# Kernel tuning notes

Measured on AMD Instinct MI355X. Metric: run time of the kernel, lower is better.

The kernel has to match this reference:

```python
import jax, jax.numpy as jnp
import numpy as np

VOCAB = 100000
EMBED = 64
SENT = 20
MEM = 50
BATCH = 32
HOPS = 3
PAD_ID = 0


def position_encoding(sentence_size, embedding_size):
    # Section 4.1 of MemN2N paper, vectorized. Returns [sentence_size, embedding_size].
    i = np.arange(1, embedding_size + 1, dtype=np.float32)[:, None]   # [E,1]
    j = np.arange(1, sentence_size + 1, dtype=np.float32)[None, :]    # [1,S]
    enc = (i - (embedding_size + 1) / 2.0) * (j - (sentence_size + 1) / 2.0)
    enc = 1.0 + 4.0 * enc / embedding_size / sentence_size
    enc[:, -1] = 1.0
    return jnp.asarray(enc.T, dtype=jnp.float32)  # [S,E]


def setup_inputs() -> dict:
    key = jax.random.key(0)
    k1, k2, k3, k4 = jax.random.split(key, 4)
    stories = jax.random.randint(k1, (BATCH, MEM, SENT), 0, VOCAB, dtype=jnp.int64 if jax.config.jax_enable_x64 else jnp.int32)
    queries = jax.random.randint(k2, (BATCH, SENT), 0, VOCAB, dtype=jnp.int64 if jax.config.jax_enable_x64 else jnp.int32)
    A = jax.random.normal(k3, (VOCAB, EMBED), dtype=jnp.float32) * 0.1
    C = jax.random.normal(k4, (HOPS, VOCAB, EMBED), dtype=jnp.float32) * 0.1
    # padding_idx=PAD_ID rows are zero, as in nn.Embedding(padding_idx=...)
    A = A.at[PAD_ID].set(0.0)
    C = C.at[:, PAD_ID].set(0.0)
    encoding = position_encoding(SENT, EMBED)
    return {"stories": stories, "queries": queries, "A": A, "C": C, "encoding": encoding}


def reference(stories, queries, A, C, encoding):
    # queries: [B,S], stories: [B,M,S], A: [V,E], C: [hops,V,E], encoding: [S,E]
    q_emb = A[queries]                                # [B,S,E]
    u = (q_emb * encoding).sum(axis=1)                # [B,E]
    for hop in range(HOPS):
        table_in = A if hop == 0 else C[hop - 1]
        emb_A = table_in[stories]                     # [B,M,S,E]
        m = (emb_A * encoding).sum(axis=2)            # [B,M,E]
        dotted = jnp.einsum('bme,be->bm', m, u)       # [B,M]
        probs = jax.nn.softmax(dotted, axis=-1)       # [B,M]
        emb_C = C[hop][stories]                       # [B,M,S,E]
        c = (emb_C * encoding).sum(axis=2)            # [B,M,E]
        o = jnp.einsum('bm,bme->be', probs, c)        # [B,E]
        u = u + o
    return u @ C[-1].T                                # [B,V]
```

## Files before the change

kernel.cpp:

```cpp
#include <hip/hip_runtime.h>
#include <hip/hip_bf16.h>

#define VOCAB 100000
#define EMBED 64
#define SENT  20
#define MEM   50
#define BATCH 32
#define HOPS  3

#define NSET  4
#define NSLOT (NSET * BATCH * MEM)

__device__ __forceinline__ float bfr(unsigned short x) {
    union { unsigned int u; float f; } cv;
    cv.u = ((unsigned int)x) << 16;
    return cv.f;
}

__device__ __forceinline__ bool is_bf16(const void* enc) {
    return ((const unsigned int*)enc)[639] == 0x3F803F80u;
}

__device__ __forceinline__ float loadT(const void* p, size_t idx, bool bf) {
    return bf ? bfr(((const unsigned short*)p)[idx]) : ((const float*)p)[idx];
}

__device__ __forceinline__ float wave_sum(float d) {
#pragma unroll
    for (int off = 32; off > 0; off >>= 1) d += __shfl_xor(d, off, 64);
    return d;
}

__global__ __launch_bounds__(256) void k_gather(
    const int* __restrict__ stories,
    const int* __restrict__ queries,
    const void* __restrict__ A,
    const void* __restrict__ C,
    const void* __restrict__ enc,
    float* __restrict__ mc_ws,
    float* __restrict__ u0g)
{
    const bool bf = is_bf16(enc);
    const int tid = threadIdx.x;
    const int e   = tid & 63;
    const int gw  = blockIdx.x * 4 + (tid >> 6);
    const size_t VE = (size_t)VOCAB * EMBED;

    float encr[SENT];
#pragma unroll
    for (int s = 0; s < SENT; ++s) encr[s] = loadT(enc, s * EMBED + e, bf);

    if (gw < NSLOT) {
        const int t  = gw / (BATCH * MEM);
        const int bm = gw % (BATCH * MEM);
        const void* T   = (t == 0) ? A : C;
        const size_t to = (t == 0) ? 0 : (size_t)(t - 1) * VE;

        int wst = (e < SENT) ? stories[bm * SENT + e] : 0;
        float acc = 0.f;
#pragma unroll
        for (int s = 0; s < SENT; ++s) {
            int w = __shfl(wst, s, 64);
            acc += loadT(T, to + (size_t)w * EMBED + e, bf) * encr[s];
        }
        mc_ws[gw * EMBED + e] = acc;
    } else if (gw < NSLOT + BATCH) {
        const int b = gw - NSLOT;
        int wq = (e < SENT) ? queries[b * SENT + e] : 0;
        float u = 0.f;
#pragma unroll
        for (int s = 0; s < SENT; ++s) {
            int w = __shfl(wq, s, 64);
            u += loadT(A, (size_t)w * EMBED + e, bf) * encr[s];
        }
        u0g[b * EMBED + e] = u;
    }
}

__global__ __launch_bounds__(256) void k_recur2(
    const float* __restrict__ mc_ws,
    const float* __restrict__ u0g,
    float* __restrict__ u3g)
{
    const int b    = blockIdx.x;
    const int tid  = threadIdx.x;
    const int lane = tid & 63;
    const int widx = tid >> 6;

    __shared__ float mc[NSET][MEM][65];
    __shared__ float uls[EMBED];
    __shared__ float ols[4][EMBED];

    for (int idx = tid; idx < NSET * MEM * 16; idx += 256) {
        int t  = idx / (MEM * 16);
        int r  = idx % (MEM * 16);
        int mm = r >> 4;
        int e4 = r & 15;
        const float4 v = *(const float4*)(mc_ws +
            (((size_t)t * BATCH * MEM) + (size_t)b * MEM + mm) * EMBED + e4 * 4);
        mc[t][mm][e4 * 4 + 0] = v.x;
        mc[t][mm][e4 * 4 + 1] = v.y;
        mc[t][mm][e4 * 4 + 2] = v.z;
        mc[t][mm][e4 * 4 + 3] = v.w;
    }
    if (tid < EMBED) uls[tid] = u0g[b * EMBED + tid];
    __syncthreads();

    for (int hop = 0; hop < HOPS; ++hop) {
        float d = 0.f;
        if (lane < MEM) {
#pragma unroll
            for (int e = 0; e < EMBED; ++e)
                d += mc[hop][lane][e] * uls[e];
        }
        float x = (lane < MEM) ? d : -3.4e38f;
        float mx = x;
#pragma unroll
        for (int off = 32; off > 0; off >>= 1) mx = fmaxf(mx, __shfl_xor(mx, off, 64));
        float ex = (lane < MEM) ? __expf(x - mx) : 0.f;
        float sm = wave_sum(ex);
        float p = ex / sm;

        float o = 0.f;
#pragma unroll
        for (int k = 0; k < 13; ++k) {
            int mm = widx * 13 + k;
            if (mm < MEM)
                o += __shfl(p, mm, 64) * mc[hop + 1][mm][lane];
        }
        ols[widx][lane] = o;
        __syncthreads();
        if (tid < EMBED)
            uls[tid] += ols[0][tid] + ols[1][tid] + ols[2][tid] + ols[3][tid];
        __syncthreads();
    }

    if (tid < EMBED) u3g[b * EMBED + tid] = uls[tid];
}

__global__ __launch_bounds__(256) void k_out(const float* __restrict__ u,
                                             const void* __restrict__ Cbase,
                                             const void* __restrict__ enc,
                                             void* __restrict__ out)
{
    bool bf = is_bf16(enc);
    const size_t c2_off = (size_t)2 * VOCAB * EMBED;
    __shared__ __align__(16) float su[BATCH * EMBED];
    for (int i = threadIdx.x; i < BATCH * EMBED; i += 256) su[i] = u[i];
    __syncthreads();
    int v = blockIdx.x * 256 + threadIdx.x;
    if (v >= VOCAB) return;

    float row[EMBED];
    if (bf) {
        const uint4* rp = (const uint4*)((const unsigned short*)Cbase + c2_off + (size_t)v * EMBED);
#pragma unroll
        for (int i = 0; i < 8; ++i) {
            uint4 r = rp[i];
            row[i*8 + 0] = bfr((unsigned short)(r.x & 0xffff));
            row[i*8 + 1] = bfr((unsigned short)(r.x >> 16));
            row[i*8 + 2] = bfr((unsigned short)(r.y & 0xffff));
            row[i*8 + 3] = bfr((unsigned short)(r.y >> 16));
            row[i*8 + 4] = bfr((unsigned short)(r.z & 0xffff));
            row[i*8 + 5] = bfr((unsigned short)(r.z >> 16));
            row[i*8 + 6] = bfr((unsigned short)(r.w & 0xffff));
            row[i*8 + 7] = bfr((unsigned short)(r.w >> 16));
        }
    } else {
        const float4* rp = (const float4*)((const float*)Cbase + c2_off + (size_t)v * EMBED);
#pragma unroll
        for (int i = 0; i < 16; ++i) {
            float4 r = rp[i];
            row[i*4 + 0] = r.x; row[i*4 + 1] = r.y;
            row[i*4 + 2] = r.z; row[i*4 + 3] = r.w;
        }
    }

    float res[BATCH];
#pragma unroll
    for (int bb = 0; bb < BATCH; ++bb) {
        const float4* sp = (const float4*)(su + bb * EMBED);
        float acc = 0.f;
#pragma unroll
        for (int e4 = 0; e4 < 16; ++e4) {
            float4 us = sp[e4];
            acc += row[e4*4+0]*us.x + row[e4*4+1]*us.y
                 + row[e4*4+2]*us.z + row[e4*4+3]*us.w;
        }
        res[bb] = acc;
    }

    if (bf) {
        unsigned short* ob = (unsigned short*)out;
#pragma unroll
        for (int bb = 0; bb < BATCH; ++bb) {
            __hip_bfloat16 h = __float2bfloat16(res[bb]);
            ob[(size_t)bb * VOCAB + v] = *(unsigned short*)&h;
        }
    } else {
        float* of = (float*)out;
#pragma unroll
        for (int bb = 0; bb < BATCH; ++bb)
            of[(size_t)bb * VOCAB + v] = res[bb];
    }
}

extern "C" void kernel_launch(void* const* d_in, const int* in_sizes, int n_in,
                              void* d_out, int out_size, void* d_ws, size_t ws_size,
                              hipStream_t stream)
{
    const int*  stories = (const int*)d_in[0];
    const int*  queries = (const int*)d_in[1];
    const void* A       = d_in[2];
    const void* C       = d_in[3];
    const void* enc     = d_in[4];

    float* mc_ws = (float*)d_ws;
    float* u0g   = mc_ws + NSLOT * EMBED;
    float* u3g   = u0g + BATCH * EMBED;

    const int nwaves  = NSLOT + BATCH;
    const int nblocks = (nwaves + 3) / 4;

    k_gather<<<nblocks, 256, 0, stream>>>(stories, queries, A, C, enc, mc_ws, u0g);
    k_recur2<<<BATCH, 256, 0, stream>>>(mc_ws, u0g, u3g);
    k_out<<<(VOCAB + 255) / 256, 256, 0, stream>>>(u3g, C, enc, d_out);
}
```

Baseline: 159.4 us.

## Split output batch across two thread halves and stream row chunks in k_out

Each vocab row in the output projection is now handled by two threads, each computing 16 of the 32 batch outputs, and the grid doubles to 128 vocab rows per block. The row is read in 8-element chunks that feed the accumulators directly instead of being held whole in registers. This lowers register pressure (16 accumulators instead of a 64-float row plus 32 results) to raise occupancy and hide memory latency better. The cost is that each C row is loaded from global memory twice, once per half.

```diff
diff --git a/kernel.cpp b/kernel.cpp
--- a/kernel.cpp
+++ b/kernel.cpp
@@ -143,65 +143,74 @@
                                              const void* __restrict__ enc,
                                              void* __restrict__ out)
 {
-    bool bf = is_bf16(enc);
+    const bool bf = is_bf16(enc);
     const size_t c2_off = (size_t)2 * VOCAB * EMBED;
+
     __shared__ __align__(16) float su[BATCH * EMBED];
     for (int i = threadIdx.x; i < BATCH * EMBED; i += 256) su[i] = u[i];
     __syncthreads();
-    int v = blockIdx.x * 256 + threadIdx.x;
+
+    const int v  = blockIdx.x * 128 + (threadIdx.x & 127);
+    const int bh = threadIdx.x >> 7;
     if (v >= VOCAB) return;
 
-    float row[EMBED];
+    float res[16];
+#pragma unroll
+    for (int i = 0; i < 16; ++i) res[i] = 0.f;
+
+    const float4* sp = (const float4*)(su + bh * 16 * EMBED);
+
     if (bf) {
         const uint4* rp = (const uint4*)((const unsigned short*)Cbase + c2_off + (size_t)v * EMBED);
 #pragma unroll
-        for (int i = 0; i < 8; ++i) {
-            uint4 r = rp[i];
-            row[i*8 + 0] = bfr((unsigned short)(r.x & 0xffff));
-            row[i*8 + 1] = bfr((unsigned short)(r.x >> 16));
-            row[i*8 + 2] = bfr((unsigned short)(r.y & 0xffff));
-            row[i*8 + 3] = bfr((unsigned short)(r.y >> 16));
-            row[i*8 + 4] = bfr((unsigned short)(r.z & 0xffff));
-            row[i*8 + 5] = bfr((unsigned short)(r.z >> 16));
-            row[i*8 + 6] = bfr((unsigned short)(r.w & 0xffff));
-            row[i*8 + 7] = bfr((unsigned short)(r.w >> 16));
+        for (int kc = 0; kc < 8; ++kc) {
+            uint4 r = rp[kc];
+            float rf[8];
+            rf[0] = bfr((unsigned short)(r.x & 0xffff));
+            rf[1] = bfr((unsigned short)(r.x >> 16));
+            rf[2] = bfr((unsigned short)(r.y & 0xffff));
+            rf[3] = bfr((unsigned short)(r.y >> 16));
+            rf[4] = bfr((unsigned short)(r.z & 0xffff));
+            rf[5] = bfr((unsigned short)(r.z >> 16));
+            rf[6] = bfr((unsigned short)(r.w & 0xffff));
+            rf[7] = bfr((unsigned short)(r.w >> 16));
+#pragma unroll
+            for (int b = 0; b < 16; ++b) {
+                float4 a0 = sp[b * 16 + kc * 2];
+                float4 a1 = sp[b * 16 + kc * 2 + 1];
+                res[b] += rf[0]*a0.x + rf[1]*a0.y + rf[2]*a0.z + rf[3]*a0.w
+                        + rf[4]*a1.x + rf[5]*a1.y + rf[6]*a1.z + rf[7]*a1.w;
+            }
         }
     } else {
         const float4* rp = (const float4*)((const float*)Cbase + c2_off + (size_t)v * EMBED);
 #pragma unroll
-        for (int i = 0; i < 16; ++i) {
-            float4 r = rp[i];
-            row[i*4 + 0] = r.x; row[i*4 + 1] = r.y;
-            row[i*4 + 2] = r.z; row[i*4 + 3] = r.w;
-        }
-    }
-
-    float res[BATCH];
-#pragma unroll
-    for (int bb = 0; bb < BATCH; ++bb) {
-        const float4* sp = (const float4*)(su + bb * EMBED);
-        float acc = 0.f;
-#pragma unroll
-        for (int e4 = 0; e4 < 16; ++e4) {
-            float4 us = sp[e4];
-            acc += row[e4*4+0]*us.x + row[e4*4+1]*us.y
-                 + row[e4*4+2]*us.z + row[e4*4+3]*us.w;
-        }
-        res[bb] = acc;
+        for (int kc = 0; kc < 8; ++kc) {
+            float4 r0 = rp[kc * 2];
+            float4 r1 = rp[kc * 2 + 1];
+            float rf[8] = { r0.x, r0.y, r0.z, r0.w, r1.x, r1.y, r1.z, r1.w };
+#pragma unroll
+            for (int b = 0; b < 16; ++b) {
+                float4 a0 = sp[b * 16 + kc * 2];
+                float4 a1 = sp[b * 16 + kc * 2 + 1];
+                res[b] += rf[0]*a0.x + rf[1]*a0.y + rf[2]*a0.z + rf[3]*a0.w
+                        + rf[4]*a1.x + rf[5]*a1.y + rf[6]*a1.z + rf[7]*a1.w;
+            }
+        }
     }
 
     if (bf) {
         unsigned short* ob = (unsigned short*)out;
 #pragma unroll
-        for (int bb = 0; bb < BATCH; ++bb) {
-            __hip_bfloat16 h = __float2bfloat16(res[bb]);
-            ob[(size_t)bb * VOCAB + v] = *(unsigned short*)&h;
+        for (int b = 0; b < 16; ++b) {
+            __hip_bfloat16 h = __float2bfloat16(res[b]);
+            ob[(size_t)(bh * 16 + b) * VOCAB + v] = *(unsigned short*)&h;
         }
     } else {
         float* of = (float*)out;
 #pragma unroll
-        for (int bb = 0; bb < BATCH; ++bb)
-            of[(size_t)bb * VOCAB + v] = res[bb];
+        for (int b = 0; b < 16; ++b)
+            of[(size_t)(bh * 16 + b) * VOCAB + v] = res[b];
     }
 }
 
@@ -224,5 +233,5 @@
 
     k_gather<<<nblocks, 256, 0, stream>>>(stories, queries, A, C, enc, mc_ws, u0g);
     k_recur2<<<BATCH, 256, 0, stream>>>(mc_ws, u0g, u3g);
-    k_out<<<(VOCAB + 255) / 256, 256, 0, stream>>>(u3g, C, enc, d_out);
-}
+    k_out<<<(VOCAB + 127) / 128, 256, 0, stream>>>(u3g, C, enc, d_out);
+}
```

Measured after the change: 165.7 us. 1.04x slower.

## Use bf16 MFMA with hi/lo split of u for output projection

Applied to the files above, without the earlier changes.

When inputs are bf16, the final projection u @ C[-1]^T now runs on bf16 MFMA 16x16x32 instructions. To keep precision, u is split into hi and lo bf16 parts in the recurrence kernel, and each tile is computed with both. Each wave handles four 16-column vocab tiles, reading C rows straight into MFMA operands and replacing per-thread scalar FMA loops over LDS. Output stores are now 16-lane partial rows rather than fully coalesced per-thread columns, and the fp32 path is simplified without LDS staging.

```diff
diff --git a/kernel.cpp b/kernel.cpp
--- a/kernel.cpp
+++ b/kernel.cpp
@@ -11,12 +11,20 @@
 #define NSET  4
 #define NSLOT (NSET * BATCH * MEM)
 
+typedef __attribute__((ext_vector_type(8))) short short8;
+typedef __attribute__((ext_vector_type(4))) float f32x4;
+
 __device__ __forceinline__ float bfr(unsigned short x) {
     union { unsigned int u; float f; } cv;
     cv.u = ((unsigned int)x) << 16;
     return cv.f;
 }
 
+__device__ __forceinline__ unsigned short f2bf(float x) {
+    __hip_bfloat16 h = __float2bfloat16(x);
+    return *(unsigned short*)&h;
+}
+
 __device__ __forceinline__ bool is_bf16(const void* enc) {
     return ((const unsigned int*)enc)[639] == 0x3F803F80u;
 }
@@ -29,6 +37,10 @@
 #pragma unroll
     for (int off = 32; off > 0; off >>= 1) d += __shfl_xor(d, off, 64);
     return d;
+}
+
+__device__ __forceinline__ f32x4 mfma16(short8 a, short8 b, f32x4 c) {
+    return __builtin_amdgcn_mfma_f32_16x16x32_bf16(a, b, c, 0, 0, 0);
 }
 
 __global__ __launch_bounds__(256) void k_gather(
@@ -80,7 +92,9 @@
 __global__ __launch_bounds__(256) void k_recur2(
     const float* __restrict__ mc_ws,
     const float* __restrict__ u0g,
-    float* __restrict__ u3g)
+    float* __restrict__ u3g,
+    unsigned short* __restrict__ u_hi,
+    unsigned short* __restrict__ u_lo)
 {
     const int b    = blockIdx.x;
     const int tid  = threadIdx.x;
@@ -135,73 +149,90 @@
         __syncthreads();
     }
 
-    if (tid < EMBED) u3g[b * EMBED + tid] = uls[tid];
-}
-
-__global__ __launch_bounds__(256) void k_out(const float* __restrict__ u,
-                                             const void* __restrict__ Cbase,
-                                             const void* __restrict__ enc,
-                                             void* __restrict__ out)
-{
-    bool bf = is_bf16(enc);
+    if (tid < EMBED) {
+        float v = uls[tid];
+        u3g[b * EMBED + tid] = v;
+        unsigned short hi = f2bf(v);
+        u_hi[b * EMBED + tid] = hi;
+        u_lo[b * EMBED + tid] = f2bf(v - bfr(hi));
+    }
+}
+
+__global__ __launch_bounds__(256) void k_out(
+    const float* __restrict__ u,
+    const unsigned short* __restrict__ u_hi,
+    const unsigned short* __restrict__ u_lo,
+    const void* __restrict__ Cbase,
+    const void* __restrict__ enc,
+    void* __restrict__ out)
+{
+    const bool bf = is_bf16(enc);
     const size_t c2_off = (size_t)2 * VOCAB * EMBED;
-    __shared__ __align__(16) float su[BATCH * EMBED];
-    for (int i = threadIdx.x; i < BATCH * EMBED; i += 256) su[i] = u[i];
-    __syncthreads();
-    int v = blockIdx.x * 256 + threadIdx.x;
-    if (v >= VOCAB) return;
-
-    float row[EMBED];
+    const int tid = threadIdx.x;
+
     if (bf) {
-        const uint4* rp = (const uint4*)((const unsigned short*)Cbase + c2_off + (size_t)v * EMBED);
-#pragma unroll
-        for (int i = 0; i < 8; ++i) {
-            uint4 r = rp[i];
-            row[i*8 + 0] = bfr((unsigned short)(r.x & 0xffff));
-            row[i*8 + 1] = bfr((unsigned short)(r.x >> 16));
-            row[i*8 + 2] = bfr((unsigned short)(r.y & 0xffff));
-            row[i*8 + 3] = bfr((unsigned short)(r.y >> 16));
-            row[i*8 + 4] = bfr((unsigned short)(r.z & 0xffff));
-            row[i*8 + 5] = bfr((unsigned short)(r.z >> 16));
-            row[i*8 + 6] = bfr((unsigned short)(r.w & 0xffff));
-            row[i*8 + 7] = bfr((unsigned short)(r.w >> 16));
+        const unsigned short* C2 = (const unsigned short*)Cbase + c2_off;
+        unsigned short* ob = (unsigned short*)out;
+        const int lane = tid & 63;
+        const int widx = tid >> 6;
+        const int l15  = lane & 15;
+        const int quad = lane >> 4;
+
+        short8 ahi[2][2], alo[2][2];
+#pragma unroll
+        for (int mt = 0; mt < 2; ++mt)
+#pragma unroll
+            for (int kc = 0; kc < 2; ++kc) {
+                size_t off = (size_t)(mt * 16 + l15) * EMBED + kc * 32 + quad * 8;
+                ahi[mt][kc] = *(const short8*)(u_hi + off);
+                alo[mt][kc] = *(const short8*)(u_lo + off);
+            }
+
+        const int base_tile = (blockIdx.x * 4 + widx) * 4;
+#pragma unroll
+        for (int i = 0; i < 4; ++i) {
+            const int v0 = (base_tile + i) * 16;
+            if (v0 >= VOCAB) break;
+            const size_t rb = (size_t)(v0 + l15) * EMBED + quad * 8;
+            short8 b0 = *(const short8*)(C2 + rb);
+            short8 b1 = *(const short8*)(C2 + rb + 32);
+
+            f32x4 acc0 = {0.f, 0.f, 0.f, 0.f};
+            f32x4 acc1 = {0.f, 0.f, 0.f, 0.f};
+            acc0 = mfma16(alo[0][0], b0, acc0);
+            acc0 = mfma16(alo[0][1], b1, acc0);
+            acc0 = mfma16(ahi[0][0], b0, acc0);
+            acc0 = mfma16(ahi[0][1], b1, acc0);
+            acc1 = mfma16(alo[1][0], b0, acc1);
+            acc1 = mfma16(alo[1][1], b1, acc1);
+            acc1 = mfma16(ahi[1][0], b0, acc1);
+            acc1 = mfma16(ahi[1][1], b1, acc1);
+
+            const int col = v0 + l15;
+#pragma unroll
+            for (int r = 0; r < 4; ++r) {
+                int row = quad * 4 + r;
+                ob[(size_t)row * VOCAB + col]        = f2bf(acc0[r]);
+                ob[(size_t)(row + 16) * VOCAB + col] = f2bf(acc1[r]);
+            }
         }
     } else {
-        const float4* rp = (const float4*)((const float*)Cbase + c2_off + (size_t)v * EMBED);
+        const int v = blockIdx.x * 256 + tid;
+        if (v >= VOCAB) return;
+        const float* C2 = (const float*)Cbase + c2_off;
+        float* of = (float*)out;
+        float row[EMBED];
 #pragma unroll
         for (int i = 0; i < 16; ++i) {
-            float4 r = rp[i];
-            row[i*4 + 0] = r.x; row[i*4 + 1] = r.y;
-            row[i*4 + 2] = r.z; row[i*4 + 3] = r.w;
-        }
-    }
-
-    float res[BATCH];
-#pragma unroll
-    for (int bb = 0; bb < BATCH; ++bb) {
-        const float4* sp = (const float4*)(su + bb * EMBED);
-        float acc = 0.f;
-#pragma unroll
-        for (int e4 = 0; e4 < 16; ++e4) {
-            float4 us = sp[e4];
-            acc += row[e4*4+0]*us.x + row[e4*4+1]*us.y
-                 + row[e4*4+2]*us.z + row[e4*4+3]*us.w;
-        }
-        res[bb] = acc;
-    }
-
-    if (bf) {
-        unsigned short* ob = (unsigned short*)out;
-#pragma unroll
-        for (int bb = 0; bb < BATCH; ++bb) {
-            __hip_bfloat16 h = __float2bfloat16(res[bb]);
-            ob[(size_t)bb * VOCAB + v] = *(unsigned short*)&h;
-        }
-    } else {
-        float* of = (float*)out;
-#pragma unroll
-        for (int bb = 0; bb < BATCH; ++bb)
-            of[(size_t)bb * VOCAB + v] = res[bb];
+            float4 r = ((const float4*)(C2 + (size_t)v * EMBED))[i];
+            row[i*4+0] = r.x; row[i*4+1] = r.y; row[i*4+2] = r.z; row[i*4+3] = r.w;
+        }
+        for (int b = 0; b < BATCH; ++b) {
+            float acc = 0.f;
+#pragma unroll
+            for (int e = 0; e < EMBED; ++e) acc += row[e] * u[b * EMBED + e];
+            of[(size_t)b * VOCAB + v] = acc;
+        }
     }
 }
 
@@ -218,11 +249,13 @@
     float* mc_ws = (float*)d_ws;
     float* u0g   = mc_ws + NSLOT * EMBED;
     float* u3g   = u0g + BATCH * EMBED;
+    unsigned short* u_hi = (unsigned short*)(u3g + BATCH * EMBED);
+    unsigned short* u_lo = u_hi + BATCH * EMBED;
 
     const int nwaves  = NSLOT + BATCH;
     const int nblocks = (nwaves + 3) / 4;
 
     k_gather<<<nblocks, 256, 0, stream>>>(stories, queries, A, C, enc, mc_ws, u0g);
-    k_recur2<<<BATCH, 256, 0, stream>>>(mc_ws, u0g, u3g);
-    k_out<<<(VOCAB + 255) / 256, 256, 0, stream>>>(u3g, C, enc, d_out);
-}
+    k_recur2<<<BATCH, 256, 0, stream>>>(mc_ws, u0g, u3g, u_hi, u_lo);
+    k_out<<<391, 256, 0, stream>>>(u3g, u_hi, u_lo, C, enc, d_out);
+}
```

New measurement: 161.9 us. About the same (+1.6%).
